# Kernel tuning notes

Measured on AMD Instinct MI355X. Metric: run time of the kernel, lower is better.

The kernel has to match this reference:

```python
import jax, jax.numpy as jnp
import numpy as np

TAU = 1.0
EPS_NORM = 1e-12  # matches F.normalize default eps
EPS_POS = 1e-5


def setup_inputs() -> dict:
    key = jax.random.key(0)
    kf, kl = jax.random.split(key)
    B, D, NUM_CLASSES = 4096, 128, 1000
    features = jax.random.normal(kf, (B, D), dtype=jnp.float32)
    labels = jax.random.randint(kl, (B,), 0, NUM_CLASSES, dtype=jnp.int64)
    return {"features": features, "labels": labels}


def reference(features, labels):
    B = features.shape[0]
    # cosine similarity via GEMM on L2-normalized features
    norm = jnp.linalg.norm(features, axis=-1, keepdims=True)
    f = features / jnp.maximum(norm, EPS_NORM)
    sim = f @ f.T  # [B, B]
    diag = jnp.eye(B, dtype=bool)
    sim = jnp.where(diag, -jnp.inf, sim)
    # log-softmax over rows at temperature tau; then zero the diagonal
    logp = jax.nn.log_softmax(sim / TAU, axis=-1)
    logp = jnp.where(diag, 0.0, logp)
    # positive-pair mask (same label, excluding self)
    mask = (labels[:, None] == labels[None, :]) & ~diag
    maskf = mask.astype(jnp.float32)
    num_pos = maskf.sum(axis=-1)  # [B]
    pos_sum = (logp * maskf).sum(axis=-1)  # [B]
    loss = -(pos_sum / (num_pos + EPS_POS)).sum() / B
    return loss
```

## Files before the change

### kernel.cpp

```cpp
#include <hip/hip_runtime.h>
#include <math.h>

#define NB 4096
#define ND 128
#define TT 256
#define NT (NB / TT)

typedef __bf16 bf16x8 __attribute__((ext_vector_type(8)));
typedef __bf16 bf16x4 __attribute__((ext_vector_type(4)));
typedef float  f32x4  __attribute__((ext_vector_type(4)));

__global__ __launch_bounds__(256) void rownorm_kernel(
    const float* __restrict__ f, __bf16* __restrict__ fnb, float* __restrict__ out)
{
    if (blockIdx.x == 0 && threadIdx.x == 0) out[0] = 0.f;
    const int t   = blockIdx.x * 256 + threadIdx.x;
    const int row = t >> 5;
    const int c   = (t & 31) << 2;
    float4 v = *reinterpret_cast<const float4*>(f + (size_t)row * ND + c);
    float ss = v.x * v.x + v.y * v.y + v.z * v.z + v.w * v.w;
#pragma unroll
    for (int off = 1; off < 32; off <<= 1) ss += __shfl_xor(ss, off, 64);
    const float inv = 1.0f / fmaxf(sqrtf(ss), 1e-12f);
    bf16x4 o;
    o[0] = (__bf16)(v.x * inv); o[1] = (__bf16)(v.y * inv);
    o[2] = (__bf16)(v.z * inv); o[3] = (__bf16)(v.w * inv);
    *reinterpret_cast<bf16x4*>(fnb + (size_t)row * ND + c) = o;
}

__global__ __launch_bounds__(512, 2) void supcon_mfma(
    const __bf16* __restrict__ fn, const int* __restrict__ labels,
    float* __restrict__ partials)
{
    __shared__ __align__(16) __bf16 At[TT * ND];
    __shared__ __align__(16) __bf16 Bt[TT * ND];
    __shared__ float redL[2][TT][3];

    const int t    = threadIdx.x;
    const int lane = t & 63;
    const int wid  = t >> 6;
    const int wr   = wid >> 1;
    const int wc   = wid & 1;
    const int bi   = blockIdx.x >> 4;
    const int cs   = blockIdx.x & 15;
    const int lr   = lane & 15;
    const int lk   = lane >> 4;
    const int ib   = bi * TT;
    const int jb   = cs * TT;

    {
        const __bf16* gA = fn + (size_t)ib * ND;
        const __bf16* gB = fn + (size_t)jb * ND;
#pragma unroll
        for (int i = 0; i < 8; ++i) {
            const int id  = i * 512 + t;
            const int row = id >> 4;
            const int c16 = id & 15;
            const int dst = (row * 16 + (c16 ^ (row & 15))) * 8;
            *reinterpret_cast<bf16x8*>(&At[dst]) =
                *reinterpret_cast<const bf16x8*>(gA + row * ND + c16 * 8);
            *reinterpret_cast<bf16x8*>(&Bt[dst]) =
                *reinterpret_cast<const bf16x8*>(gB + row * ND + c16 * 8);
        }
    }

    int ig[4], labi[4];
#pragma unroll
    for (int it = 0; it < 4; ++it) {
        ig[it]   = ib + wr * 64 + it * 16 + lr;
        labi[it] = labels[ig[it]];
    }

    __syncthreads();

    bf16x8 bfr[4][4];
#pragma unroll
    for (int it = 0; it < 4; ++it)
#pragma unroll
        for (int ks = 0; ks < 4; ++ks) {
            const int row = wr * 64 + it * 16 + lr;
            bfr[it][ks] = *reinterpret_cast<const bf16x8*>(
                &At[(row * 16 + ((ks * 4 + lk) ^ lr)) * 8]);
        }

    float es[4] = {}, ps[4] = {}, np[4] = {};

#pragma unroll
    for (int jt = 0; jt < 8; ++jt) {
        bf16x8 af[4];
#pragma unroll
        for (int ks = 0; ks < 4; ++ks) {
            const int row = wc * 128 + jt * 16 + lr;
            af[ks] = *reinterpret_cast<const bf16x8*>(
                &Bt[(row * 16 + ((ks * 4 + lk) ^ lr)) * 8]);
        }
        f32x4 acc[4] = {};
#pragma unroll
        for (int ks = 0; ks < 4; ++ks)
#pragma unroll
            for (int it = 0; it < 4; ++it)
                acc[it] = __builtin_amdgcn_mfma_f32_16x16x32_bf16(af[ks], bfr[it][ks], acc[it], 0, 0, 0);

        const int jg0 = jb + wc * 128 + jt * 16 + lk * 4;
        const int4 lj4 = *reinterpret_cast<const int4*>(&labels[jg0]);
        const int lj[4] = {lj4.x, lj4.y, lj4.z, lj4.w};

#pragma unroll
        for (int it = 0; it < 4; ++it)
#pragma unroll
            for (int r = 0; r < 4; ++r) {
                const int   jgv  = jg0 + r;
                const float s    = acc[it][r];
                const float e    = __expf(s);
                const bool  self = (jgv == ig[it]);
                const bool  pos  = (lj[r] == labi[it]) && !self;
                es[it] += self ? 0.f : e;
                ps[it] += pos ? s : 0.f;
                np[it] += pos ? 1.f : 0.f;
            }
    }

#pragma unroll
    for (int off = 16; off < 64; off <<= 1)
#pragma unroll
        for (int it = 0; it < 4; ++it) {
            es[it] += __shfl_xor(es[it], off, 64);
            ps[it] += __shfl_xor(ps[it], off, 64);
            np[it] += __shfl_xor(np[it], off, 64);
        }
    if (lk == 0) {
#pragma unroll
        for (int it = 0; it < 4; ++it) {
            const int rl = wr * 64 + it * 16 + lr;
            redL[wc][rl][0] = es[it];
            redL[wc][rl][1] = ps[it];
            redL[wc][rl][2] = np[it];
        }
    }
    __syncthreads();
    if (t < TT) {
        float* p = partials + ((size_t)cs * NB + ib + t) * 3;
        p[0] = redL[0][t][0] + redL[1][t][0];
        p[1] = redL[0][t][1] + redL[1][t][1];
        p[2] = redL[0][t][2] + redL[1][t][2];
    }
}

__global__ __launch_bounds__(256) void final_kernel(
    const float* __restrict__ partials, float* __restrict__ out)
{
    const int row = blockIdx.x * 256 + threadIdx.x;
    float es = 0.f, ps = 0.f, np = 0.f;
#pragma unroll
    for (int cs = 0; cs < NT; ++cs) {
        const float* p = partials + ((size_t)cs * NB + row) * 3;
        es += p[0]; ps += p[1]; np += p[2];
    }
    const float lse = logf(es);
    float c = -(ps - np * lse) / ((np + 1e-5f) * (float)NB);
#pragma unroll
    for (int off = 1; off < 64; off <<= 1) c += __shfl_xor(c, off, 64);
    __shared__ float sred[4];
    if ((threadIdx.x & 63) == 0) sred[threadIdx.x >> 6] = c;
    __syncthreads();
    if (threadIdx.x == 0) atomicAdd(out, sred[0] + sred[1] + sred[2] + sred[3]);
}

extern "C" void kernel_launch(void* const* d_in, const int* in_sizes, int n_in,
                              void* d_out, int out_size, void* d_ws, size_t ws_size,
                              hipStream_t stream) {
    const float* features = (const float*)d_in[0];
    const int*   labels   = (const int*)d_in[1];
    float* out = (float*)d_out;

    __bf16* fnb      = (__bf16*)d_ws;
    float*  partials = (float*)((char*)d_ws + (size_t)NB * ND * 2);

    rownorm_kernel<<<NB * 32 / 256, 256, 0, stream>>>(features, fnb, out);
    supcon_mfma<<<NT * NT, 512, 0, stream>>>(fnb, labels, partials);
    final_kernel<<<NB / 256, 256, 0, stream>>>(partials, out);
}
```

Measured before the change: 21.79 us.

## Fuse row normalization into MFMA kernel and widen blocks to 1024 threads

Removes the separate rownorm kernel: each tile block now loads fp32 features, computes row L2 norms with shuffles, and writes normalized bf16 into swizzled LDS directly. Block size doubles to 16 waves, each covering 64 columns instead of 128, so per-wave work halves. This saves one launch and the bf16 round trip through global memory. In exchange every row is normalized 16 times across blocks, more fp32 data is read, and the larger blocks change occupancy.

```diff
diff --git a/kernel.cpp b/kernel.cpp
--- a/kernel.cpp
+++ b/kernel.cpp
@@ -7,40 +7,21 @@
 #define NT (NB / TT)
 
 typedef __bf16 bf16x8 __attribute__((ext_vector_type(8)));
-typedef __bf16 bf16x4 __attribute__((ext_vector_type(4)));
 typedef float  f32x4  __attribute__((ext_vector_type(4)));
 
-__global__ __launch_bounds__(256) void rownorm_kernel(
-    const float* __restrict__ f, __bf16* __restrict__ fnb, float* __restrict__ out)
-{
-    if (blockIdx.x == 0 && threadIdx.x == 0) out[0] = 0.f;
-    const int t   = blockIdx.x * 256 + threadIdx.x;
-    const int row = t >> 5;
-    const int c   = (t & 31) << 2;
-    float4 v = *reinterpret_cast<const float4*>(f + (size_t)row * ND + c);
-    float ss = v.x * v.x + v.y * v.y + v.z * v.z + v.w * v.w;
-#pragma unroll
-    for (int off = 1; off < 32; off <<= 1) ss += __shfl_xor(ss, off, 64);
-    const float inv = 1.0f / fmaxf(sqrtf(ss), 1e-12f);
-    bf16x4 o;
-    o[0] = (__bf16)(v.x * inv); o[1] = (__bf16)(v.y * inv);
-    o[2] = (__bf16)(v.z * inv); o[3] = (__bf16)(v.w * inv);
-    *reinterpret_cast<bf16x4*>(fnb + (size_t)row * ND + c) = o;
-}
-
-__global__ __launch_bounds__(512, 2) void supcon_mfma(
-    const __bf16* __restrict__ fn, const int* __restrict__ labels,
-    float* __restrict__ partials)
+__global__ __launch_bounds__(1024) void supcon_mfma(
+    const float* __restrict__ f, const int* __restrict__ labels,
+    float* __restrict__ partials, float* __restrict__ out)
 {
     __shared__ __align__(16) __bf16 At[TT * ND];
     __shared__ __align__(16) __bf16 Bt[TT * ND];
-    __shared__ float redL[2][TT][3];
+    __shared__ float redL[4][TT][3];
 
     const int t    = threadIdx.x;
     const int lane = t & 63;
     const int wid  = t >> 6;
-    const int wr   = wid >> 1;
-    const int wc   = wid & 1;
+    const int wr   = wid >> 2;
+    const int wc   = wid & 3;
     const int bi   = blockIdx.x >> 4;
     const int cs   = blockIdx.x & 15;
     const int lr   = lane & 15;
@@ -48,19 +29,34 @@
     const int ib   = bi * TT;
     const int jb   = cs * TT;
 
+    if (blockIdx.x == 0 && t == 0) out[0] = 0.f;
+
     {
-        const __bf16* gA = fn + (size_t)ib * ND;
-        const __bf16* gB = fn + (size_t)jb * ND;
+        const int c16  = t & 15;
+        const int rloc = t >> 4;
+        const float* gA = f + (size_t)ib * ND;
+        const float* gB = f + (size_t)jb * ND;
 #pragma unroll
-        for (int i = 0; i < 8; ++i) {
-            const int id  = i * 512 + t;
-            const int row = id >> 4;
-            const int c16 = id & 15;
-            const int dst = (row * 16 + (c16 ^ (row & 15))) * 8;
-            *reinterpret_cast<bf16x8*>(&At[dst]) =
-                *reinterpret_cast<const bf16x8*>(gA + row * ND + c16 * 8);
-            *reinterpret_cast<bf16x8*>(&Bt[dst]) =
-                *reinterpret_cast<const bf16x8*>(gB + row * ND + c16 * 8);
+        for (int s = 0; s < 2; ++s) {
+            const float* g = s ? gB : gA;
+            __bf16*      T = s ? Bt : At;
+#pragma unroll
+            for (int p = 0; p < 4; ++p) {
+                const int row = p * 64 + rloc;
+                const float4 lo = *reinterpret_cast<const float4*>(g + row * ND + c16 * 8);
+                const float4 hi = *reinterpret_cast<const float4*>(g + row * ND + c16 * 8 + 4);
+                float ss = lo.x*lo.x + lo.y*lo.y + lo.z*lo.z + lo.w*lo.w
+                         + hi.x*hi.x + hi.y*hi.y + hi.z*hi.z + hi.w*hi.w;
+#pragma unroll
+                for (int off = 1; off < 16; off <<= 1) ss += __shfl_xor(ss, off, 64);
+                const float inv = 1.0f / fmaxf(sqrtf(ss), 1e-12f);
+                bf16x8 o;
+                o[0] = (__bf16)(lo.x * inv); o[1] = (__bf16)(lo.y * inv);
+                o[2] = (__bf16)(lo.z * inv); o[3] = (__bf16)(lo.w * inv);
+                o[4] = (__bf16)(hi.x * inv); o[5] = (__bf16)(hi.y * inv);
+                o[6] = (__bf16)(hi.z * inv); o[7] = (__bf16)(hi.w * inv);
+                *reinterpret_cast<bf16x8*>(&T[(row * 16 + (c16 ^ (row & 15))) * 8]) = o;
+            }
         }
     }
 
@@ -86,11 +82,11 @@
     float es[4] = {}, ps[4] = {}, np[4] = {};
 
 #pragma unroll
-    for (int jt = 0; jt < 8; ++jt) {
+    for (int jt = 0; jt < 4; ++jt) {
         bf16x8 af[4];
 #pragma unroll
         for (int ks = 0; ks < 4; ++ks) {
-            const int row = wc * 128 + jt * 16 + lr;
+            const int row = wc * 64 + jt * 16 + lr;
             af[ks] = *reinterpret_cast<const bf16x8*>(
                 &Bt[(row * 16 + ((ks * 4 + lk) ^ lr)) * 8]);
         }
@@ -99,9 +95,10 @@
         for (int ks = 0; ks < 4; ++ks)
 #pragma unroll
             for (int it = 0; it < 4; ++it)
-                acc[it] = __builtin_amdgcn_mfma_f32_16x16x32_bf16(af[ks], bfr[it][ks], acc[it], 0, 0, 0);
+                acc[it] = __builtin_amdgcn_mfma_f32_16x16x32_bf16(
+                    af[ks], bfr[it][ks], acc[it], 0, 0, 0);
 
-        const int jg0 = jb + wc * 128 + jt * 16 + lk * 4;
+        const int jg0 = jb + wc * 64 + jt * 16 + lk * 4;
         const int4 lj4 = *reinterpret_cast<const int4*>(&labels[jg0]);
         const int lj[4] = {lj4.x, lj4.y, lj4.z, lj4.w};
 
@@ -140,9 +137,9 @@
     __syncthreads();
     if (t < TT) {
         float* p = partials + ((size_t)cs * NB + ib + t) * 3;
-        p[0] = redL[0][t][0] + redL[1][t][0];
-        p[1] = redL[0][t][1] + redL[1][t][1];
-        p[2] = redL[0][t][2] + redL[1][t][2];
+        p[0] = redL[0][t][0] + redL[1][t][0] + redL[2][t][0] + redL[3][t][0];
+        p[1] = redL[0][t][1] + redL[1][t][1] + redL[2][t][1] + redL[3][t][1];
+        p[2] = redL[0][t][2] + redL[1][t][2] + redL[2][t][2] + redL[3][t][2];
     }
 }
 
@@ -172,11 +169,8 @@
     const float* features = (const float*)d_in[0];
     const int*   labels   = (const int*)d_in[1];
     float* out = (float*)d_out;
+    float* partials = (float*)d_ws;
 
-    __bf16* fnb      = (__bf16*)d_ws;
-    float*  partials = (float*)((char*)d_ws + (size_t)NB * ND * 2);
-
-    rownorm_kernel<<<NB * 32 / 256, 256, 0, stream>>>(features, fnb, out);
-    supcon_mfma<<<NT * NT, 512, 0, stream>>>(fnb, labels, partials);
+    supcon_mfma<<<NT * NT, 1024, 0, stream>>>(features, labels, partials, out);
     final_kernel<<<NB / 256, 256, 0, stream>>>(partials, out);
 }
```

Measured after the change: 29.53 us. 35.5% more time.
